# Kernel optimization log

Hardware: AMD Instinct MI355X
Metric: run time of the kernel (lower is better)

Reference implementation:

```python
import jax, jax.numpy as jnp
import numpy as np

N_NODES = 100000
N_EDGES = 1000000
H = 128  # hidden_size


def setup_inputs() -> dict:
    key = jax.random.key(0)
    ks = jax.random.split(key, 8)
    emb = jax.random.normal(ks[0], (N_NODES, H), dtype=jnp.float32)
    edge_index = jax.random.randint(ks[1], (2, N_EDGES), 0, N_NODES, dtype=jnp.int64)
    # MLP([2H, 4H, H, 1]) weights (Kaiming-ish scaled normals)
    W1 = jax.random.normal(ks[2], (2 * H, 4 * H), dtype=jnp.float32) / np.sqrt(2 * H).astype(np.float32)
    b1 = jnp.zeros((4 * H,), dtype=jnp.float32)
    W2 = jax.random.normal(ks[3], (4 * H, H), dtype=jnp.float32) / np.sqrt(4 * H).astype(np.float32)
    b2 = jnp.zeros((H,), dtype=jnp.float32)
    W3 = jax.random.normal(ks[4], (H, 1), dtype=jnp.float32) / np.sqrt(H).astype(np.float32)
    b3 = jnp.zeros((1,), dtype=jnp.float32)
    return {"emb": emb, "edge_index": edge_index,
            "W1": W1, "b1": b1, "W2": W2, "b2": b2, "W3": W3, "b3": b3}


def reference(emb, edge_index, W1, b1, W2, b2, W3, b3):
    # ExtractorMLP.forward with learn_edge_att=True, eval mode.
    col = edge_index[0]
    row = edge_index[1]
    # edge-gather + concat: [E, 2H]
    f12 = jnp.concatenate([emb[col], emb[row]], axis=-1)
    # MLP([2H, 4H, H, 1]); Dropout is identity in eval mode
    h = jax.nn.relu(f12 @ W1 + b1)          # [E, 4H]
    h = jax.nn.relu(h @ W2 + b2)            # [E, H]
    att_log_logits = h @ W3 + b3            # [E, 1]
    # concrete_sample with training=False -> plain sigmoid
    att = jax.nn.sigmoid(att_log_logits)
    return att
```

## Files before the change

### kernel.cpp

```cpp
#include <hip/hip_runtime.h>
#include <math.h>

#define E_TOTAL   1000000
#define HDIM      128
#define K1        256
#define N1        512
#define N2        128
#define M_TILE    64
#define BLOCK     256

typedef _Float16 f16;
typedef _Float16 f16_4  __attribute__((ext_vector_type(4)));
typedef _Float16 f16_8  __attribute__((ext_vector_type(8)));
typedef float    f32_16 __attribute__((ext_vector_type(16)));

__global__ void prep_weights(const float* __restrict__ W1, const float* __restrict__ W2,
                             f16* __restrict__ W1F, f16* __restrict__ W2F) {
    int t = blockIdx.x * blockDim.x + threadIdx.x;
    const int total1 = K1 * N1;
    const int total2 = N1 * N2;
    if (t < total1) {
        int v    = t & 7;
        int lane = (t >> 3) & 63;
        int kc   = (t >> 9) & 15;
        int nt   = t >> 13;
        int k = kc * 16 + (lane >> 5) * 8 + v;
        int n = nt * 32 + (lane & 31);
        W1F[t] = (f16)W1[k * N1 + n];
    } else if (t < total1 + total2) {
        int u = t - total1;
        int v    = u & 7;
        int lane = (u >> 3) & 63;
        int kcg  = (u >> 9) & 31;
        int nt   = u >> 14;
        int k = kcg * 16 + (lane >> 5) * 8 + v;
        int n = nt * 32 + (lane & 31);
        W2F[u] = (f16)W2[k * N2 + n];
    }
}

__global__ void prep_emb(const float* __restrict__ emb, f16* __restrict__ emb16) {
    int t = blockIdx.x * blockDim.x + threadIdx.x;
    float4 f = ((const float4*)emb)[t];
    f16_4 v = { (f16)f.x, (f16)f.y, (f16)f.z, (f16)f.w };
    ((f16_4*)emb16)[t] = v;
}

template <bool F16EMB>
__global__ __launch_bounds__(BLOCK, 2) void edge_mlp_kernel(
    const float* __restrict__ emb,
    const f16*   __restrict__ emb16,
    const int*   __restrict__ eidx,
    const f16*   __restrict__ W1F,
    const float* __restrict__ b1,
    const f16*   __restrict__ W2F,
    const float* __restrict__ b2,
    const float* __restrict__ W3,
    const float* __restrict__ b3,
    float* __restrict__ out)
{
    __shared__ __align__(16) f16 sAF[2 * 16 * 64 * 8];
    __shared__ __align__(16) f16 sBF[2][2 * 8 * 64 * 8];
    f16* sH2F = sAF;

    const int tid = threadIdx.x;
    const int e0  = blockIdx.x * M_TILE;

    {
        const int m    = tid >> 2;
        const int side = (tid >> 1) & 1;
        const int sub  = tid & 1;
        const int met  = m >> 5;
        const int m31  = m & 31;
        const int node = eidx[side * E_TOTAL + e0 + m];
        if (F16EMB) {
            const f16* src = emb16 + (size_t)node * HDIM;
            #pragma unroll
            for (int j = 0; j < 4; ++j) {
                const int g = side * 8 + sub * 4 + j;
                const int koff = (sub * 4 + j) * 16;
                #pragma unroll
                for (int lh = 0; lh < 2; ++lh) {
                    f16_8 v = *(const f16_8*)(src + koff + lh * 8);
                    *(f16_8*)(sAF + (((met * 16 + g) * 64 + lh * 32 + m31) << 3)) = v;
                }
            }
        } else {
            const float* src = emb + (size_t)node * HDIM;
            #pragma unroll
            for (int j = 0; j < 4; ++j) {
                const int g = side * 8 + sub * 4 + j;
                const int koff = (sub * 4 + j) * 16;
                #pragma unroll
                for (int lh = 0; lh < 2; ++lh) {
                    float4 fa = *(const float4*)(src + koff + lh * 8);
                    float4 fb = *(const float4*)(src + koff + lh * 8 + 4);
                    f16_8 v = { (f16)fa.x, (f16)fa.y, (f16)fa.z, (f16)fa.w,
                                (f16)fb.x, (f16)fb.y, (f16)fb.z, (f16)fb.w };
                    *(f16_8*)(sAF + (((met * 16 + g) * 64 + lh * 32 + m31) << 3)) = v;
                }
            }
        }
    }
    __syncthreads();

    const int wnt  = tid >> 6;
    const int lane = tid & 63;
    const int l31  = lane & 31;
    const int lh   = lane >> 5;

    f32_16 acc2[2] = {{0.f}, {0.f}};

    {
        f32_16 acc1[2] = {{0.f}, {0.f}};
        const int nt = wnt;
        #pragma unroll
        for (int kc = 0; kc < 16; ++kc) {
            f16_8 wf = *(const f16_8*)(W1F + (((nt * 16 + kc) * 64 + lane) << 3));
            #pragma unroll
            for (int et = 0; et < 2; ++et) {
                f16_8 ef = *(const f16_8*)(sAF + (((et * 16 + kc) * 64 + lane) << 3));
                acc1[et] = __builtin_amdgcn_mfma_f32_32x32x16_f16(wf, ef, acc1[et], 0, 0, 0);
            }
        }
        f16* bcur = &sBF[0][0];
        #pragma unroll
        for (int et = 0; et < 2; ++et) {
            #pragma unroll
            for (int g = 0; g < 4; ++g) {
                const int wnl = wnt * 32 + lh * 4 + g * 8;
                const float4 bv = *(const float4*)(b1 + wnl);
                f16_4 hv;
                #pragma unroll
                for (int i = 0; i < 4; ++i) {
                    float v = acc1[et][g * 4 + i] + ((const float*)&bv)[i];
                    hv[i] = (f16)(v > 0.f ? v : 0.f);
                }
                const int kl = wnt * 2 + (g >> 1);
                *(f16_4*)(bcur + ((((et * 8 + kl) * 64 + (g & 1) * 32 + l31) << 3) + lh * 4)) = hv;
            }
        }
    }
    __syncthreads();

    #pragma unroll
    for (int q = 1; q < 4; ++q) {
        f32_16 acc1[2] = {{0.f}, {0.f}};
        const int nt = q * 4 + wnt;
        const f16* bprev = &sBF[(q - 1) & 1][0];
        #pragma unroll
        for (int kc = 0; kc < 16; ++kc) {
            f16_8 wf = *(const f16_8*)(W1F + (((nt * 16 + kc) * 64 + lane) << 3));
            #pragma unroll
            for (int et = 0; et < 2; ++et) {
                f16_8 ef = *(const f16_8*)(sAF + (((et * 16 + kc) * 64 + lane) << 3));
                acc1[et] = __builtin_amdgcn_mfma_f32_32x32x16_f16(wf, ef, acc1[et], 0, 0, 0);
            }
            if (kc < 8) {
                const int kcg = (q - 1) * 8 + kc;
                f16_8 wf2 = *(const f16_8*)(W2F + (((wnt * 32 + kcg) * 64 + lane) << 3));
                #pragma unroll
                for (int et = 0; et < 2; ++et) {
                    f16_8 ef2 = *(const f16_8*)(bprev + (((et * 8 + kc) * 64 + lane) << 3));
                    acc2[et] = __builtin_amdgcn_mfma_f32_32x32x16_f16(wf2, ef2, acc2[et], 0, 0, 0);
                }
            }
        }
        f16* bcur = &sBF[q & 1][0];
        #pragma unroll
        for (int et = 0; et < 2; ++et) {
            #pragma unroll
            for (int g = 0; g < 4; ++g) {
                const int wnl = wnt * 32 + lh * 4 + g * 8;
                const float4 bv = *(const float4*)(b1 + q * 128 + wnl);
                f16_4 hv;
                #pragma unroll
                for (int i = 0; i < 4; ++i) {
                    float v = acc1[et][g * 4 + i] + ((const float*)&bv)[i];
                    hv[i] = (f16)(v > 0.f ? v : 0.f);
                }
                const int kl = wnt * 2 + (g >> 1);
                *(f16_4*)(bcur + ((((et * 8 + kl) * 64 + (g & 1) * 32 + l31) << 3) + lh * 4)) = hv;
            }
        }
        __syncthreads();
    }

    {
        const f16* bprev = &sBF[1][0];
        #pragma unroll
        for (int kc = 0; kc < 8; ++kc) {
            const int kcg = 24 + kc;
            f16_8 wf2 = *(const f16_8*)(W2F + (((wnt * 32 + kcg) * 64 + lane) << 3));
            #pragma unroll
            for (int et = 0; et < 2; ++et) {
                f16_8 ef2 = *(const f16_8*)(bprev + (((et * 8 + kc) * 64 + lane) << 3));
                acc2[et] = __builtin_amdgcn_mfma_f32_32x32x16_f16(wf2, ef2, acc2[et], 0, 0, 0);
            }
        }
    }

    {
        #pragma unroll
        for (int et = 0; et < 2; ++et) {
            #pragma unroll
            for (int g = 0; g < 4; ++g) {
                const int wn = wnt * 32 + lh * 4 + g * 8;
                const float4 bv = *(const float4*)(b2 + wn);
                f16_4 hv;
                #pragma unroll
                for (int i = 0; i < 4; ++i) {
                    float v = acc2[et][g * 4 + i] + ((const float*)&bv)[i];
                    hv[i] = (f16)(v > 0.f ? v : 0.f);
                }
                const int kl = wnt * 2 + (g >> 1);
                *(f16_4*)(sH2F + ((((et * 8 + kl) * 64 + (g & 1) * 32 + l31) << 3) + lh * 4)) = hv;
            }
        }
    }
    __syncthreads();

    {
        const int m   = tid >> 2;
        const int j   = tid & 3;
        const int met = m >> 5;
        const int m31 = m & 31;
        float s = 0.f;
        #pragma unroll
        for (int jj = 0; jj < 2; ++jj) {
            const int kl = j * 2 + jj;
            f16_8 a = *(const f16_8*)(sH2F + (((met * 8 + kl) * 64 + m31) << 3));
            f16_8 b = *(const f16_8*)(sH2F + (((met * 8 + kl) * 64 + 32 + m31) << 3));
            const float4* w3v = (const float4*)(W3 + kl * 16);
            float4 w0 = w3v[0], w1 = w3v[1], w2 = w3v[2], w3q = w3v[3];
            s += (float)a[0]*w0.x + (float)a[1]*w0.y + (float)a[2]*w0.z + (float)a[3]*w0.w;
            s += (float)a[4]*w1.x + (float)a[5]*w1.y + (float)a[6]*w1.z + (float)a[7]*w1.w;
            s += (float)b[0]*w2.x + (float)b[1]*w2.y + (float)b[2]*w2.z + (float)b[3]*w2.w;
            s += (float)b[4]*w3q.x + (float)b[5]*w3q.y + (float)b[6]*w3q.z + (float)b[7]*w3q.w;
        }
        s += __shfl_xor(s, 1);
        s += __shfl_xor(s, 2);
        if (j == 0) {
            const float logit = s + b3[0];
            out[e0 + m] = 1.0f / (1.0f + __expf(-logit));
        }
    }
}

extern "C" void kernel_launch(void* const* d_in, const int* in_sizes, int n_in,
                              void* d_out, int out_size, void* d_ws, size_t ws_size,
                              hipStream_t stream) {
    const float* emb  = (const float*)d_in[0];
    const int*   eidx = (const int*)d_in[1];
    const float* W1   = (const float*)d_in[2];
    const float* b1   = (const float*)d_in[3];
    const float* W2   = (const float*)d_in[4];
    const float* b2   = (const float*)d_in[5];
    const float* W3   = (const float*)d_in[6];
    const float* b3   = (const float*)d_in[7];
    float* out = (float*)d_out;

    const size_t wbytes   = (size_t)(K1 * N1 + N1 * N2) * sizeof(f16);
    const size_t embbytes = (size_t)100000 * HDIM * sizeof(f16);

    f16* W1F = (f16*)d_ws;
    f16* W2F = W1F + K1 * N1;

    const int prep_total = K1 * N1 + N1 * N2;
    prep_weights<<<(prep_total + 255) / 256, 256, 0, stream>>>(W1, W2, W1F, W2F);

    if (ws_size >= wbytes + embbytes) {
        f16* emb16 = W2F + N1 * N2;
        const int cvt_threads = 100000 * HDIM / 4;
        prep_emb<<<cvt_threads / 256, 256, 0, stream>>>(emb, emb16);
        edge_mlp_kernel<true><<<E_TOTAL / M_TILE, BLOCK, 0, stream>>>(
            emb, emb16, eidx, W1F, b1, W2F, b2, W3, b3, out);
    } else {
        edge_mlp_kernel<false><<<E_TOTAL / M_TILE, BLOCK, 0, stream>>>(
            emb, (const f16*)nullptr, eidx, W1F, b1, W2F, b2, W3, b3, out);
    }
}
```

Baseline: 575.7 us.

## Gather edge embeddings directly into registers instead of staging through LDS

Each wave now loads its gathered embedding fragments (32 f16x8 vectors per lane) straight from global memory into registers in MFMA operand layout. This removes the shared-memory A tile, its staging writes, the per-k-chunk LDS reads and one block barrier, and shrinks LDS use. In exchange, all four waves redundantly gather the same edge rows from global/L2, and register pressure rises by 128 VGPRs per lane, which may cause spills or lower occupancy under launch_bounds(256,2).

Measured after the change: 663.5 us. 1.15x slower.

```diff
diff --git a/kernel.cpp b/kernel.cpp
--- a/kernel.cpp
+++ b/kernel.cpp
@@ -59,56 +59,47 @@
     const float* __restrict__ b3,
     float* __restrict__ out)
 {
-    __shared__ __align__(16) f16 sAF[2 * 16 * 64 * 8];
     __shared__ __align__(16) f16 sBF[2][2 * 8 * 64 * 8];
-    f16* sH2F = sAF;
-
-    const int tid = threadIdx.x;
-    const int e0  = blockIdx.x * M_TILE;
-
-    {
-        const int m    = tid >> 2;
-        const int side = (tid >> 1) & 1;
-        const int sub  = tid & 1;
-        const int met  = m >> 5;
-        const int m31  = m & 31;
-        const int node = eidx[side * E_TOTAL + e0 + m];
-        if (F16EMB) {
-            const f16* src = emb16 + (size_t)node * HDIM;
-            #pragma unroll
-            for (int j = 0; j < 4; ++j) {
-                const int g = side * 8 + sub * 4 + j;
-                const int koff = (sub * 4 + j) * 16;
-                #pragma unroll
-                for (int lh = 0; lh < 2; ++lh) {
-                    f16_8 v = *(const f16_8*)(src + koff + lh * 8);
-                    *(f16_8*)(sAF + (((met * 16 + g) * 64 + lh * 32 + m31) << 3)) = v;
-                }
-            }
-        } else {
-            const float* src = emb + (size_t)node * HDIM;
-            #pragma unroll
-            for (int j = 0; j < 4; ++j) {
-                const int g = side * 8 + sub * 4 + j;
-                const int koff = (sub * 4 + j) * 16;
-                #pragma unroll
-                for (int lh = 0; lh < 2; ++lh) {
-                    float4 fa = *(const float4*)(src + koff + lh * 8);
-                    float4 fb = *(const float4*)(src + koff + lh * 8 + 4);
-                    f16_8 v = { (f16)fa.x, (f16)fa.y, (f16)fa.z, (f16)fa.w,
-                                (f16)fb.x, (f16)fb.y, (f16)fb.z, (f16)fb.w };
-                    *(f16_8*)(sAF + (((met * 16 + g) * 64 + lh * 32 + m31) << 3)) = v;
-                }
-            }
-        }
-    }
-    __syncthreads();
-
+    __shared__ __align__(16) f16 sH2F[2 * 8 * 64 * 8];
+
+    const int tid  = threadIdx.x;
+    const int e0   = blockIdx.x * M_TILE;
     const int wnt  = tid >> 6;
     const int lane = tid & 63;
     const int l31  = lane & 31;
     const int lh   = lane >> 5;
 
+    int node[2][2];
+    #pragma unroll
+    for (int et = 0; et < 2; ++et)
+        #pragma unroll
+        for (int side = 0; side < 2; ++side)
+            node[et][side] = eidx[side * E_TOTAL + e0 + et * 32 + l31];
+
+    f16_8 ef[2][16];
+    if (F16EMB) {
+        #pragma unroll
+        for (int et = 0; et < 2; ++et)
+            #pragma unroll
+            for (int kc = 0; kc < 16; ++kc) {
+                const f16* src = emb16 + (size_t)node[et][kc >> 3] * HDIM
+                                       + (kc & 7) * 16 + lh * 8;
+                ef[et][kc] = *(const f16_8*)src;
+            }
+    } else {
+        #pragma unroll
+        for (int et = 0; et < 2; ++et)
+            #pragma unroll
+            for (int kc = 0; kc < 16; ++kc) {
+                const float* src = emb + (size_t)node[et][kc >> 3] * HDIM
+                                       + (kc & 7) * 16 + lh * 8;
+                float4 fa = *(const float4*)(src);
+                float4 fb = *(const float4*)(src + 4);
+                ef[et][kc] = { (f16)fa.x, (f16)fa.y, (f16)fa.z, (f16)fa.w,
+                               (f16)fb.x, (f16)fb.y, (f16)fb.z, (f16)fb.w };
+            }
+    }
+
     f32_16 acc2[2] = {{0.f}, {0.f}};
 
     {
@@ -118,10 +109,8 @@
         for (int kc = 0; kc < 16; ++kc) {
             f16_8 wf = *(const f16_8*)(W1F + (((nt * 16 + kc) * 64 + lane) << 3));
             #pragma unroll
-            for (int et = 0; et < 2; ++et) {
-                f16_8 ef = *(const f16_8*)(sAF + (((et * 16 + kc) * 64 + lane) << 3));
-                acc1[et] = __builtin_amdgcn_mfma_f32_32x32x16_f16(wf, ef, acc1[et], 0, 0, 0);
-            }
+            for (int et = 0; et < 2; ++et)
+                acc1[et] = __builtin_amdgcn_mfma_f32_32x32x16_f16(wf, ef[et][kc], acc1[et], 0, 0, 0);
         }
         f16* bcur = &sBF[0][0];
         #pragma unroll
@@ -152,10 +141,8 @@
         for (int kc = 0; kc < 16; ++kc) {
             f16_8 wf = *(const f16_8*)(W1F + (((nt * 16 + kc) * 64 + lane) << 3));
             #pragma unroll
-            for (int et = 0; et < 2; ++et) {
-                f16_8 ef = *(const f16_8*)(sAF + (((et * 16 + kc) * 64 + lane) << 3));
-                acc1[et] = __builtin_amdgcn_mfma_f32_32x32x16_f16(wf, ef, acc1[et], 0, 0, 0);
-            }
+            for (int et = 0; et < 2; ++et)
+                acc1[et] = __builtin_amdgcn_mfma_f32_32x32x16_f16(wf, ef[et][kc], acc1[et], 0, 0, 0);
             if (kc < 8) {
                 const int kcg = (q - 1) * 8 + kc;
                 f16_8 wf2 = *(const f16_8*)(W2F + (((wnt * 32 + kcg) * 64 + lane) << 3));
```
